# Optimization experiments

Hardware: AMD Instinct MI355X
Metric: run time of the kernel (lower is better)

Reference implementation:

```python
import jax, jax.numpy as jnp
import numpy as np

B, T_IN, F, U = 4096, 256, 32, 64
OUT_STEPS = 24


def _lstm_step(x, h, c, W, R, b):
    # Keras LSTMCell: gates z = x@W + h@R + b, split as [i, f, g, o]
    z = x @ W + h @ R + b  # [B, 4U]
    i, f, g, o = jnp.split(z, 4, axis=-1)
    i = jax.nn.sigmoid(i)
    f = jax.nn.sigmoid(f)
    g = jnp.tanh(g)
    o = jax.nn.sigmoid(o)
    c_new = f * c + i * g
    h_new = o * jnp.tanh(c_new)
    return h_new, c_new


def setup_inputs() -> dict:
    key = jax.random.key(0)
    ks = jax.random.split(key, 9)
    s_in = 1.0 / np.sqrt(F)
    s_hid = 1.0 / np.sqrt(U)
    return {
        "inputs": jax.random.normal(ks[0], (B, T_IN, F), jnp.float32),
        "W1": jax.random.normal(ks[1], (F, 4 * U), jnp.float32) * s_in,
        "U1": jax.random.normal(ks[2], (U, 4 * U), jnp.float32) * s_hid,
        "b1": jnp.zeros((4 * U,), jnp.float32),
        "W2": jax.random.normal(ks[3], (F, 4 * U), jnp.float32) * s_in,
        "U2": jax.random.normal(ks[4], (U, 4 * U), jnp.float32) * s_hid,
        "b2": jnp.zeros((4 * U,), jnp.float32),
        "Wd": jax.random.normal(ks[5], (U, F), jnp.float32) * s_hid,
        "bd": jnp.zeros((F,), jnp.float32),
    }


def reference(inputs, W1, U1, b1, W2, U2, b2, Wd, bd):
    batch = inputs.shape[0]
    units = U1.shape[0]
    h0 = jnp.zeros((batch, units), inputs.dtype)
    c0 = jnp.zeros((batch, units), inputs.dtype)

    # ---- warmup: run lstm_cell_warmup over the input sequence ----
    def warm_step(carry, x_t):
        h, c = carry
        h, c = _lstm_step(x_t, h, c, W1, U1, b1)
        return (h, c), None

    (h, c), _ = jax.lax.scan(warm_step, (h0, c0), jnp.swapaxes(inputs, 0, 1))
    pred0 = h @ Wd + bd  # [B, F]

    def dec_step(carry, _):
        pred, h, c = carry
        h, c = _lstm_step(pred, h, c, W2, U2, b2)
        pred = h @ Wd + bd
        return (pred, h, c), pred

    _, preds_rest = jax.lax.scan(dec_step, (pred0, h, c), None, length=OUT_STEPS - 1)
    preds = jnp.concatenate([pred0[None], preds_rest], axis=0)  # [T_out, B, F]
    return jnp.transpose(preds, (1, 0, 2))  # [B, T_out, F]
```

## Files before the change

### kernel.cpp

```cpp
#include <hip/hip_runtime.h>
#include <math.h>

#define T_STEPS 256
#define Fdim 32
#define Udim 64
#define G4 256
#define OUT_STEPS 24
#define ROWS 16
#define NBLK 256
#define NTHR 1024
#define HBS 72
#define CHUNK 32
#define NCHUNK 8
#define LOG2E 1.4426950408889634f

typedef __attribute__((ext_vector_type(8))) short short8;
typedef __attribute__((ext_vector_type(4))) float f32x4;

__device__ __forceinline__ short f2bf(float f) {
    union { float f; unsigned u; } v; v.f = f;
    unsigned r = v.u + 0x7FFFu + ((v.u >> 16) & 1u);
    return (short)(r >> 16);
}
__device__ __forceinline__ float bf2f(short s) {
    union { unsigned u; float f; } v; v.u = ((unsigned)(unsigned short)s) << 16;
    return v.f;
}
__device__ __forceinline__ float frcp(float v) { return __builtin_amdgcn_rcpf(v); }
__device__ __forceinline__ float fexp2(float v) { return __builtin_amdgcn_exp2f(v); }

__device__ __forceinline__ unsigned pkbf(float lo, float hi) {
    unsigned r;
    asm("v_cvt_pk_bf16_f32 %0, %1, %2" : "=v"(r) : "v"(lo), "v"(hi));
    return r;
}

__device__ __forceinline__ float cell_h(const f32x4 a, float& cst) {
    float A  = fexp2(-a[0]);
    float Bv = fexp2(a[2]);
    float rf = frcp(1.0f + fexp2(-a[1]));
    float ig = (Bv - 1.0f) * frcp((1.0f + A) * (1.0f + Bv));
    cst = fmaf(cst, rf, ig);
    float C  = fexp2(-a[3]);
    float D  = fexp2(2.0f * LOG2E * cst);
    return (D - 1.0f) * frcp((1.0f + C) * (1.0f + D));
}

#define BAR() asm volatile("s_waitcnt lgkmcnt(0)\n\ts_barrier" ::: "memory")

#define MFMA __builtin_amdgcn_mfma_f32_16x16x32_bf16

__global__ __launch_bounds__(NTHR, 1)
void lstm_v8(const float* __restrict__ x,
             const float* __restrict__ W1, const float* __restrict__ U1, const float* __restrict__ b1,
             const float* __restrict__ W2, const float* __restrict__ U2, const float* __restrict__ b2,
             const float* __restrict__ Wd, const float* __restrict__ bd,
             float* __restrict__ out)
{
    __shared__ __align__(16) short hb[2][ROWS][HBS];
    __shared__ __align__(16) short xs[CHUNK][ROWS][HBS];
    __shared__ float WdL[Udim * Fdim];

    const int tid = threadIdx.x;
    const int l   = tid & 63;
    const int w   = tid >> 6;
    const int q   = l >> 4;
    const int m   = l & 15;
    const int brow = blockIdx.x * ROWS;

    const int f4 = tid & 7;
    const int tt = (tid >> 3) & 31;
    const int r0 = tid >> 8;
    float4 pf[4];
#pragma unroll
    for (int i = 0; i < 4; ++i)
        pf[i] = *(const float4*)&x[((size_t)(brow + r0 + 4 * i) * T_STEPS + tt) * Fdim + f4 * 4];

    short8 wa1[3], wa2[3];
    f32x4 bs1, bs2;
    {
        const int unit_a = (w >> 1) * 8 + (m >> 2) * 2 + (w & 1);
        const int gate_a = m & 3;
        const int col = gate_a * 64 + unit_a;
        const float sA = (gate_a == 2) ? 2.0f * LOG2E : LOG2E;
#pragma unroll
        for (int kt = 0; kt < 3; ++kt) {
            short8 fa, fb;
#pragma unroll
            for (int j = 0; j < 8; ++j) {
                const int k = kt * 32 + q * 8 + j;
                float v1 = (k < Udim) ? U1[k * G4 + col] : W1[(k - Udim) * G4 + col];
                float v2 = (k < Udim) ? U2[k * G4 + col] : W2[(k - Udim) * G4 + col];
                fa[j] = f2bf(v1 * sA);
                fb[j] = f2bf(v2 * sA);
            }
            wa1[kt] = fa;
            wa2[kt] = fb;
        }
    }
    const int unit_d = (w >> 1) * 8 + q * 2 + (w & 1);
#pragma unroll
    for (int g = 0; g < 4; ++g) {
        const float sD = (g == 2) ? 2.0f * LOG2E : LOG2E;
        bs1[g] = b1[g * 64 + unit_d] * sD;
        bs2[g] = b2[g * 64 + unit_d] * sD;
    }

    const int sr = tid >> 5;
    const int sc = tid & 31;
    const float bdv = bd[sc];

    for (int idx = tid; idx < 2 * ROWS * HBS; idx += NTHR) ((short*)hb)[idx] = 0;
    for (int idx = tid; idx < Udim * Fdim; idx += NTHR) WdL[idx] = Wd[idx];
    float cst = 0.f;

    for (int c = 0; c < NCHUNK; ++c) {
#pragma unroll
        for (int i = 0; i < 4; ++i) {
            const int row = r0 + 4 * i;
            uint2 pk;
            pk.x = pkbf(pf[i].x, pf[i].y);
            pk.y = pkbf(pf[i].z, pf[i].w);
            *(uint2*)&xs[tt][row][f4 * 4] = pk;
        }
        if (c + 1 < NCHUNK) {
#pragma unroll
            for (int i = 0; i < 4; ++i)
                pf[i] = *(const float4*)&x[((size_t)(brow + r0 + 4 * i) * T_STEPS + ((c + 1) * CHUNK + tt)) * Fdim + f4 * 4];
        }
        BAR();

        short8 b2p = *(const short8*)&xs[0][m][q * 8];

#pragma unroll 2
        for (int t2 = 0; t2 < CHUNK; ++t2) {
            const int p = t2 & 1;

            const short8 b2v = b2p;
            const short8 b0  = *(const short8*)&hb[p][m][q * 8];
            const short8 b1v = *(const short8*)&hb[p][m][32 + q * 8];

            f32x4 a = MFMA(wa1[2], b2v, bs1, 0, 0, 0);
            a = MFMA(wa1[0], b0, a, 0, 0, 0);
            a = MFMA(wa1[1], b1v, a, 0, 0, 0);

            const float h0 = cell_h(a, cst);
            hb[1 - p][m][unit_d] = f2bf(h0);
            if (t2 + 1 < CHUNK)
                b2p = *(const short8*)&xs[t2 + 1][m][q * 8];
            BAR();
        }
    }

    short8 b0p, b1p;
    if (tid < 512) {
        float acc = bdv;
#pragma unroll
        for (int kb = 0; kb < 8; ++kb) {
            short8 h8 = *(const short8*)&hb[0][sr][kb * 8];
#pragma unroll
            for (int j = 0; j < 8; ++j)
                acc = fmaf(bf2f(h8[j]), WdL[(kb * 8 + j) * Fdim + sc], acc);
        }
        out[(size_t)(brow + sr) * (OUT_STEPS * Fdim) + sc] = acc;
        xs[0][sr][sc] = f2bf(acc);
    }
    b0p = *(const short8*)&hb[0][m][q * 8];
    b1p = *(const short8*)&hb[0][m][32 + q * 8];
    BAR();

    int dp = 0;
    for (int s = 1; s < OUT_STEPS; ++s) {
        const short8 b2v = *(const short8*)&xs[0][m][q * 8];

        f32x4 a = MFMA(wa2[0], b0p, bs2, 0, 0, 0);
        a = MFMA(wa2[1], b1p, a, 0, 0, 0);
        a = MFMA(wa2[2], b2v, a, 0, 0, 0);

        const float h0 = cell_h(a, cst);
        hb[1 - dp][m][unit_d] = f2bf(h0);
        BAR();

        if (tid < 512) {
            float dacc = bdv;
#pragma unroll
            for (int kb = 0; kb < 8; ++kb) {
                short8 h8 = *(const short8*)&hb[1 - dp][sr][kb * 8];
#pragma unroll
                for (int j = 0; j < 8; ++j)
                    dacc = fmaf(bf2f(h8[j]), WdL[(kb * 8 + j) * Fdim + sc], dacc);
            }
            out[(size_t)(brow + sr) * (OUT_STEPS * Fdim) + s * Fdim + sc] = dacc;
            xs[0][sr][sc] = f2bf(dacc);
        }
        b0p = *(const short8*)&hb[1 - dp][m][q * 8];
        b1p = *(const short8*)&hb[1 - dp][m][32 + q * 8];
        BAR();
        dp = 1 - dp;
    }
}

extern "C" void kernel_launch(void* const* d_in, const int* in_sizes, int n_in,
                              void* d_out, int out_size, void* d_ws, size_t ws_size,
                              hipStream_t stream) {
    (void)in_sizes; (void)n_in; (void)out_size; (void)d_ws; (void)ws_size;
    const float* x  = (const float*)d_in[0];
    const float* W1 = (const float*)d_in[1];
    const float* U1 = (const float*)d_in[2];
    const float* b1 = (const float*)d_in[3];
    const float* W2 = (const float*)d_in[4];
    const float* U2 = (const float*)d_in[5];
    const float* b2 = (const float*)d_in[6];
    const float* Wd = (const float*)d_in[7];
    const float* bd = (const float*)d_in[8];
    float* out = (float*)d_out;

    lstm_v8<<<dim3(NBLK), dim3(NTHR), 0, stream>>>(
        x, W1, U1, b1, W2, U2, b2, Wd, bd, out);
}
```

Measured before the change: 304.1 us.

## Shrink block to 4 waves, each computing four gate tiles per step

Cuts the block from 16 waves to 4, so each wave issues 12 independent MFMAs per step across four unit tiles and keeps four cell states in registers. Hidden-state writes are packed as two bf16 pairs, and the x staging chunk is halved to fit the smaller thread count. The aim is cheaper per-step barriers and MFMA chains that can interleave and hide latency, since the recurrence is bound by latency and barriers. The cost is more serial work per wave and higher register pressure from 24 weight fragments.

New measurement: 341.1 us. 12.1% more time.

```diff
diff --git a/kernel.cpp b/kernel.cpp
--- a/kernel.cpp
+++ b/kernel.cpp
@@ -8,10 +8,10 @@
 #define OUT_STEPS 24
 #define ROWS 16
 #define NBLK 256
-#define NTHR 1024
+#define NTHR 256
 #define HBS 72
-#define CHUNK 32
-#define NCHUNK 8
+#define CHUNK 16
+#define NCHUNK 16
 #define LOG2E 1.4426950408889634f
 
 typedef __attribute__((ext_vector_type(8))) short short8;
@@ -51,7 +51,7 @@
 #define MFMA __builtin_amdgcn_mfma_f32_16x16x32_bf16
 
 __global__ __launch_bounds__(NTHR, 1)
-void lstm_v8(const float* __restrict__ x,
+void lstm_v9(const float* __restrict__ x,
              const float* __restrict__ W1, const float* __restrict__ U1, const float* __restrict__ b1,
              const float* __restrict__ W2, const float* __restrict__ U2, const float* __restrict__ b2,
              const float* __restrict__ Wd, const float* __restrict__ bd,
@@ -69,17 +69,18 @@
     const int brow = blockIdx.x * ROWS;
 
     const int f4 = tid & 7;
-    const int tt = (tid >> 3) & 31;
-    const int r0 = tid >> 8;
-    float4 pf[4];
-#pragma unroll
-    for (int i = 0; i < 4; ++i)
-        pf[i] = *(const float4*)&x[((size_t)(brow + r0 + 4 * i) * T_STEPS + tt) * Fdim + f4 * 4];
-
-    short8 wa1[3], wa2[3];
-    f32x4 bs1, bs2;
-    {
-        const int unit_a = (w >> 1) * 8 + (m >> 2) * 2 + (w & 1);
+    const int xrow = (tid >> 3) & 15;
+    const int tb = tid >> 7;
+    float4 pf[8];
+#pragma unroll
+    for (int i = 0; i < 8; ++i)
+        pf[i] = *(const float4*)&x[((size_t)(brow + xrow) * T_STEPS + (tb + 2 * i)) * Fdim + f4 * 4];
+
+    short8 wa1[4][3], wa2[4][3];
+    f32x4 bs1[4], bs2[4];
+#pragma unroll
+    for (int i = 0; i < 4; ++i) {
+        const int unit_a = 16 * w + (i >> 1) * 8 + (m >> 2) * 2 + (i & 1);
         const int gate_a = m & 3;
         const int col = gate_a * 64 + unit_a;
         const float sA = (gate_a == 2) ? 2.0f * LOG2E : LOG2E;
@@ -94,39 +95,40 @@
                 fa[j] = f2bf(v1 * sA);
                 fb[j] = f2bf(v2 * sA);
             }
-            wa1[kt] = fa;
-            wa2[kt] = fb;
-        }
-    }
-    const int unit_d = (w >> 1) * 8 + q * 2 + (w & 1);
-#pragma unroll
-    for (int g = 0; g < 4; ++g) {
-        const float sD = (g == 2) ? 2.0f * LOG2E : LOG2E;
-        bs1[g] = b1[g * 64 + unit_d] * sD;
-        bs2[g] = b2[g * 64 + unit_d] * sD;
-    }
-
-    const int sr = tid >> 5;
-    const int sc = tid & 31;
-    const float bdv = bd[sc];
+            wa1[i][kt] = fa;
+            wa2[i][kt] = fb;
+        }
+        const int unit_d = 16 * w + (i >> 1) * 8 + q * 2 + (i & 1);
+#pragma unroll
+        for (int g = 0; g < 4; ++g) {
+            const float sD = (g == 2) ? 2.0f * LOG2E : LOG2E;
+            bs1[i][g] = b1[g * 64 + unit_d] * sD;
+            bs2[i][g] = b2[g * 64 + unit_d] * sD;
+        }
+    }
+
+    const int hw0 = 16 * w + q * 2;
+    const int hw1 = hw0 + 8;
+    const int sr = tid >> 4;
+    const int sc = tid & 15;
+    const float bdv0 = bd[sc], bdv1 = bd[sc + 16];
 
     for (int idx = tid; idx < 2 * ROWS * HBS; idx += NTHR) ((short*)hb)[idx] = 0;
     for (int idx = tid; idx < Udim * Fdim; idx += NTHR) WdL[idx] = Wd[idx];
-    float cst = 0.f;
+    float cst0 = 0.f, cst1 = 0.f, cst2 = 0.f, cst3 = 0.f;
 
     for (int c = 0; c < NCHUNK; ++c) {
 #pragma unroll
-        for (int i = 0; i < 4; ++i) {
-            const int row = r0 + 4 * i;
+        for (int i = 0; i < 8; ++i) {
             uint2 pk;
             pk.x = pkbf(pf[i].x, pf[i].y);
             pk.y = pkbf(pf[i].z, pf[i].w);
-            *(uint2*)&xs[tt][row][f4 * 4] = pk;
+            *(uint2*)&xs[tb + 2 * i][xrow][f4 * 4] = pk;
         }
         if (c + 1 < NCHUNK) {
 #pragma unroll
-            for (int i = 0; i < 4; ++i)
-                pf[i] = *(const float4*)&x[((size_t)(brow + r0 + 4 * i) * T_STEPS + ((c + 1) * CHUNK + tt)) * Fdim + f4 * 4];
+            for (int i = 0; i < 8; ++i)
+                pf[i] = *(const float4*)&x[((size_t)(brow + xrow) * T_STEPS + ((c + 1) * CHUNK + tb + 2 * i)) * Fdim + f4 * 4];
         }
         BAR();
 
@@ -140,12 +142,25 @@
             const short8 b0  = *(const short8*)&hb[p][m][q * 8];
             const short8 b1v = *(const short8*)&hb[p][m][32 + q * 8];
 
-            f32x4 a = MFMA(wa1[2], b2v, bs1, 0, 0, 0);
-            a = MFMA(wa1[0], b0, a, 0, 0, 0);
-            a = MFMA(wa1[1], b1v, a, 0, 0, 0);
-
-            const float h0 = cell_h(a, cst);
-            hb[1 - p][m][unit_d] = f2bf(h0);
+            f32x4 a0 = MFMA(wa1[0][2], b2v, bs1[0], 0, 0, 0);
+            f32x4 a1 = MFMA(wa1[1][2], b2v, bs1[1], 0, 0, 0);
+            f32x4 a2 = MFMA(wa1[2][2], b2v, bs1[2], 0, 0, 0);
+            f32x4 a3 = MFMA(wa1[3][2], b2v, bs1[3], 0, 0, 0);
+            a0 = MFMA(wa1[0][0], b0, a0, 0, 0, 0);
+            a1 = MFMA(wa1[1][0], b0, a1, 0, 0, 0);
+            a2 = MFMA(wa1[2][0], b0, a2, 0, 0, 0);
+            a3 = MFMA(wa1[3][0], b0, a3, 0, 0, 0);
+            a0 = MFMA(wa1[0][1], b1v, a0, 0, 0, 0);
+            a1 = MFMA(wa1[1][1], b1v, a1, 0, 0, 0);
+            a2 = MFMA(wa1[2][1], b1v, a2, 0, 0, 0);
+            a3 = MFMA(wa1[3][1], b1v, a3, 0, 0, 0);
+
+            const float h0 = cell_h(a0, cst0);
+            const float h1 = cell_h(a1, cst1);
+            const float h2 = cell_h(a2, cst2);
+            const float h3 = cell_h(a3, cst3);
+            *(unsigned*)&hb[1 - p][m][hw0] = pkbf(h0, h1);
+            *(unsigned*)&hb[1 - p][m][hw1] = pkbf(h2, h3);
             if (t2 + 1 < CHUNK)
                 b2p = *(const short8*)&xs[t2 + 1][m][q * 8];
             BAR();
@@ -153,45 +168,68 @@
     }
 
     short8 b0p, b1p;
-    if (tid < 512) {
-        float acc = bdv;
+    {
+        float acc0 = bdv0, acc1 = bdv1;
 #pragma unroll
         for (int kb = 0; kb < 8; ++kb) {
             short8 h8 = *(const short8*)&hb[0][sr][kb * 8];
 #pragma unroll
-            for (int j = 0; j < 8; ++j)
-                acc = fmaf(bf2f(h8[j]), WdL[(kb * 8 + j) * Fdim + sc], acc);
-        }
-        out[(size_t)(brow + sr) * (OUT_STEPS * Fdim) + sc] = acc;
-        xs[0][sr][sc] = f2bf(acc);
-    }
-    b0p = *(const short8*)&hb[0][m][q * 8];
-    b1p = *(const short8*)&hb[0][m][32 + q * 8];
+            for (int j = 0; j < 8; ++j) {
+                const float hf = bf2f(h8[j]);
+                acc0 = fmaf(hf, WdL[(kb * 8 + j) * Fdim + sc], acc0);
+                acc1 = fmaf(hf, WdL[(kb * 8 + j) * Fdim + sc + 16], acc1);
+            }
+        }
+        out[(size_t)(brow + sr) * (OUT_STEPS * Fdim) + sc] = acc0;
+        out[(size_t)(brow + sr) * (OUT_STEPS * Fdim) + sc + 16] = acc1;
+        xs[0][sr][sc] = f2bf(acc0);
+        xs[0][sr][sc + 16] = f2bf(acc1);
+        b0p = *(const short8*)&hb[0][m][q * 8];
+        b1p = *(const short8*)&hb[0][m][32 + q * 8];
+    }
     BAR();
 
     int dp = 0;
     for (int s = 1; s < OUT_STEPS; ++s) {
         const short8 b2v = *(const short8*)&xs[0][m][q * 8];
 
-        f32x4 a = MFMA(wa2[0], b0p, bs2, 0, 0, 0);
-        a = MFMA(wa2[1], b1p, a, 0, 0, 0);
-        a = MFMA(wa2[2], b2v, a, 0, 0, 0);
-
-        const float h0 = cell_h(a, cst);
-        hb[1 - dp][m][unit_d] = f2bf(h0);
+        f32x4 a0 = MFMA(wa2[0][0], b0p, bs2[0], 0, 0, 0);
+        f32x4 a1 = MFMA(wa2[1][0], b0p, bs2[1], 0, 0, 0);
+        f32x4 a2 = MFMA(wa2[2][0], b0p, bs2[2], 0, 0, 0);
+        f32x4 a3 = MFMA(wa2[3][0], b0p, bs2[3], 0, 0, 0);
+        a0 = MFMA(wa2[0][1], b1p, a0, 0, 0, 0);
+        a1 = MFMA(wa2[1][1], b1p, a1, 0, 0, 0);
+        a2 = MFMA(wa2[2][1], b1p, a2, 0, 0, 0);
+        a3 = MFMA(wa2[3][1], b1p, a3, 0, 0, 0);
+        a0 = MFMA(wa2[0][2], b2v, a0, 0, 0, 0);
+        a1 = MFMA(wa2[1][2], b2v, a1, 0, 0, 0);
+        a2 = MFMA(wa2[2][2], b2v, a2, 0, 0, 0);
+        a3 = MFMA(wa2[3][2], b2v, a3, 0, 0, 0);
+
+        const float h0 = cell_h(a0, cst0);
+        const float h1 = cell_h(a1, cst1);
+        const float h2 = cell_h(a2, cst2);
+        const float h3 = cell_h(a3, cst3);
+        *(unsigned*)&hb[1 - dp][m][hw0] = pkbf(h0, h1);
+        *(unsigned*)&hb[1 - dp][m][hw1] = pkbf(h2, h3);
         BAR();
 
-        if (tid < 512) {
-            float dacc = bdv;
+        {
+            float acc0 = bdv0, acc1 = bdv1;
 #pragma unroll
             for (int kb = 0; kb < 8; ++kb) {
                 short8 h8 = *(const short8*)&hb[1 - dp][sr][kb * 8];
 #pragma unroll
-                for (int j = 0; j < 8; ++j)
-                    dacc = fmaf(bf2f(h8[j]), WdL[(kb * 8 + j) * Fdim + sc], dacc);
+                for (int j = 0; j < 8; ++j) {
+                    const float hf = bf2f(h8[j]);
+                    acc0 = fmaf(hf, WdL[(kb * 8 + j) * Fdim + sc], acc0);
+                    acc1 = fmaf(hf, WdL[(kb * 8 + j) * Fdim + sc + 16], acc1);
+                }
             }
-            out[(size_t)(brow + sr) * (OUT_STEPS * Fdim) + s * Fdim + sc] = dacc;
-            xs[0][sr][sc] = f2bf(dacc);
+            out[(size_t)(brow + sr) * (OUT_STEPS * Fdim) + s * Fdim + sc] = acc0;
+            out[(size_t)(brow + sr) * (OUT_STEPS * Fdim) + s * Fdim + sc + 16] = acc1;
+            xs[0][sr][sc] = f2bf(acc0);
+            xs[0][sr][sc + 16] = f2bf(acc1);
         }
         b0p = *(const short8*)&hb[1 - dp][m][q * 8];
         b1p = *(const short8*)&hb[1 - dp][m][32 + q * 8];
@@ -215,6 +253,6 @@
     const float* bd = (const float*)d_in[8];
     float* out = (float*)d_out;
 
-    lstm_v8<<<dim3(NBLK), dim3(NTHR), 0, stream>>>(
+    lstm_v9<<<dim3(NBLK), dim3(NTHR), 0, stream>>>(
         x, W1, U1, b1, W2, U2, b2, Wd, bd, out);
 }
```
